# Kernel optimization log

Hardware: AMD Instinct MI355X
Metric: run time of the kernel (lower is better)

Reference implementation:

```python
import jax, jax.numpy as jnp
import numpy as np

NEG_SLOPE = 0.2

def gat_conv(x, src, dst, W, a_src, a_dst, bias, N):
    # PyG GATConv, heads=1: h = xW; e_ij = LeakyReLU(a_src.h_j + a_dst.h_i)
    h = x @ W                                   # [N, H]
    as_ = h @ a_src                             # [N]
    ad_ = h @ a_dst                             # [N]
    e = jax.nn.leaky_relu(as_[src] + ad_[dst], NEG_SLOPE)   # [E]
    m = jax.ops.segment_max(e, dst, num_segments=N)          # per-target max
    w = jnp.exp(e - m[dst])
    denom = jax.ops.segment_sum(w, dst, num_segments=N)
    alpha = w / (denom[dst] + 1e-16)                          # [E]
    out = jax.ops.segment_sum(alpha[:, None] * h[src], dst, num_segments=N)
    return out + bias


def setup_inputs() -> dict:
    key = jax.random.key(0)
    N, E, D, H, A = 20000, 320000, 256, 256, 8
    ks = jax.random.split(key, 16)
    s = lambda k, shp, fan: jax.random.normal(k, shp, jnp.float32) * (1.0 / np.sqrt(fan))
    return {
        "obs": jax.random.normal(ks[0], (N, D), jnp.float32),
        "edge_index": jax.random.randint(ks[1], (2, E), 0, N, dtype=jnp.int32),
        "W1": s(ks[2], (D, H), D), "a1_src": s(ks[3], (H,), H), "a1_dst": s(ks[4], (H,), H), "b1": jnp.zeros((H,), jnp.float32),
        "W2": s(ks[5], (H, H), H), "a2_src": s(ks[6], (H,), H), "a2_dst": s(ks[7], (H,), H), "b2": jnp.zeros((H,), jnp.float32),
        "Wm1": s(ks[8], (H, H), H), "bm1": jnp.zeros((H,), jnp.float32),
        "Wm2": s(ks[9], (H, A), H), "bm2": jnp.zeros((A,), jnp.float32),
    }


def reference(obs, edge_index, W1, a1_src, a1_dst, b1, W2, a2_src, a2_dst, b2, Wm1, bm1, Wm2, bm2):
    N = obs.shape[0]
    loops = jnp.arange(N, dtype=edge_index.dtype)
    src = jnp.concatenate([edge_index[0], loops])   # add self-loops (PyG default)
    dst = jnp.concatenate([edge_index[1], loops])
    x = jax.nn.relu(gat_conv(obs, src, dst, W1, a1_src, a1_dst, b1, N))
    x = jax.nn.relu(gat_conv(x,   src, dst, W2, a2_src, a2_dst, b2, N))
    x = jax.nn.relu(x @ Wm1 + bm1)
    return jnp.tanh(x @ Wm2 + bm2)
```

## Files before the change

### kernel.cpp

```cpp
#include <hip/hip_runtime.h>
#include <hip/hip_bf16.h>
#include <math.h>
#include <stdio.h>

typedef __attribute__((ext_vector_type(8))) short short8;
typedef __attribute__((ext_vector_type(4))) float f32x4;
typedef __attribute__((ext_vector_type(4))) unsigned short us4;
typedef __attribute__((ext_vector_type(8))) unsigned short us8;

__device__ __forceinline__ float us2f(unsigned short u) {
    return __uint_as_float(((unsigned)u) << 16);
}
__device__ __forceinline__ unsigned short f2us_rtn(float f) {
    return (unsigned short)__bfloat16_as_ushort(__float2bfloat16(f));
}

__global__ void prep_all(const float* __restrict__ Wa, const float* __restrict__ Wb,
                         const float* __restrict__ Wc, const float* __restrict__ obs,
                         unsigned short* __restrict__ TA, unsigned short* __restrict__ TB,
                         unsigned short* __restrict__ TC, unsigned short* __restrict__ obsb,
                         float* __restrict__ as1, float* __restrict__ ad1,
                         float* __restrict__ as2, float* __restrict__ ad2,
                         int* __restrict__ deg,
                         int K, int Nn, int N, int nObs8) {
    const int tot = K * Nn;
    int idx = blockIdx.x * blockDim.x + threadIdx.x;
    if (idx < 3 * tot) {
        const float* W;
        unsigned short* T;
        if (idx < tot) { W = Wa; T = TA; }
        else if (idx < 2 * tot) { W = Wb; T = TB; idx -= tot; }
        else { W = Wc; T = TC; idx -= 2 * tot; }
        const int n = idx / K, k = idx - n * K;
        T[idx] = f2us_rtn(W[(size_t)k * Nn + n]);
        return;
    }
    idx -= 3 * tot;
    if (idx < 5 * N) {
        if (idx < N) as1[idx] = 0.f;
        else if (idx < 2 * N) ad1[idx - N] = 0.f;
        else if (idx < 3 * N) as2[idx - 2 * N] = 0.f;
        else if (idx < 4 * N) ad2[idx - 3 * N] = 0.f;
        else deg[idx - 4 * N] = 0;
        return;
    }
    idx -= 5 * N;
    if (idx < nObs8) {
        const float4 a = *(const float4*)(obs + (size_t)idx * 8);
        const float4 b = *(const float4*)(obs + (size_t)idx * 8 + 4);
        const float f[8] = {a.x, a.y, a.z, a.w, b.x, b.y, b.z, b.w};
        short8 o;
#pragma unroll
        for (int e = 0; e < 8; e++) o[e] = (short)f2us_rtn(f[e]);
        *(short8*)(obsb + (size_t)idx * 8) = o;
    }
}

#define LP 72
__global__ __launch_bounds__(256) void gemm_mfma(const unsigned short* __restrict__ A,
                                                 const unsigned short* __restrict__ Bt,
                                                 const float* __restrict__ avs,
                                                 const float* __restrict__ avd,
                                                 float* __restrict__ as_,
                                                 float* __restrict__ ad_,
                                                 unsigned short* __restrict__ C,
                                                 int M, int Nn, int K) {
    __shared__ unsigned short sA[64 * LP];
    __shared__ unsigned short sB[128 * LP];
    const int tid = threadIdx.x;
    const int wave = tid >> 6, lane = tid & 63;
    const int m16 = lane & 15, quad = lane >> 4;
    const int row0 = blockIdx.x * 64, col0 = blockIdx.y * 128;
    const int wr = (wave >> 1) * 32, wc = (wave & 1) * 64;
    const int ar = tid >> 2, akc = (tid & 3) * 8;
    const int bkc = (tid & 7) * 8, bcb = tid >> 3;
    const int gr = (row0 + ar) < M ? (row0 + ar) : (M - 1);
    const unsigned short* Arow = A + (size_t)gr * K + akc;
    const unsigned short* Bcol = Bt + (size_t)(col0 + bcb) * K + bkc;

    short8 rA0, rA1, rb0, rb1, rb2, rb3;
    auto LOADT = [&](int k0) {
        rA0 = *(const short8*)(Arow + k0);
        rA1 = *(const short8*)(Arow + k0 + 32);
        rb0 = *(const short8*)(Bcol + k0);
        rb1 = *(const short8*)(Bcol + (size_t)32 * K + k0);
        rb2 = *(const short8*)(Bcol + (size_t)64 * K + k0);
        rb3 = *(const short8*)(Bcol + (size_t)96 * K + k0);
    };
    auto STORET = [&]() {
        *(short8*)&sA[ar * LP + akc]      = rA0;
        *(short8*)&sA[ar * LP + akc + 32] = rA1;
        *(short8*)&sB[bcb * LP + bkc]        = rb0;
        *(short8*)&sB[(bcb + 32) * LP + bkc] = rb1;
        *(short8*)&sB[(bcb + 64) * LP + bkc] = rb2;
        *(short8*)&sB[(bcb + 96) * LP + bkc] = rb3;
    };

    f32x4 acc[2][4] = {};
    LOADT(0);
    STORET();
    __syncthreads();
    for (int k0 = 0; k0 < K; k0 += 64) {
        const bool more = (k0 + 64) < K;
        if (more) LOADT(k0 + 64);
#pragma unroll
        for (int ks = 0; ks < 2; ks++) {
            short8 ah[2];
#pragma unroll
            for (int mi = 0; mi < 2; mi++)
                ah[mi] = *(const short8*)&sA[(wr + mi * 16 + m16) * LP + ks * 32 + quad * 8];
#pragma unroll
            for (int ni = 0; ni < 4; ni++) {
                const short8 bv = *(const short8*)&sB[(wc + ni * 16 + m16) * LP + ks * 32 + quad * 8];
#pragma unroll
                for (int mi = 0; mi < 2; mi++)
                    acc[mi][ni] = __builtin_amdgcn_mfma_f32_16x16x32_bf16(ah[mi], bv, acc[mi][ni], 0, 0, 0);
            }
        }
        __syncthreads();
        if (more) { STORET(); __syncthreads(); }
    }
    float ps[2][4] = {}, pd[2][4] = {};
#pragma unroll
    for (int mi = 0; mi < 2; mi++) {
        const int orow_base = row0 + wr + mi * 16 + quad * 4;
#pragma unroll
        for (int ni = 0; ni < 4; ni++) {
            const int ocol = col0 + wc + ni * 16 + m16;
            const float asv = avs[ocol], adv = avd[ocol];
#pragma unroll
            for (int r = 0; r < 4; r++) {
                const int orow = orow_base + r;
                if (orow < M) {
                    const float v = acc[mi][ni][r];
                    C[(size_t)orow * Nn + ocol] = f2us_rtn(v);
                    ps[mi][r] = fmaf(v, asv, ps[mi][r]);
                    pd[mi][r] = fmaf(v, adv, pd[mi][r]);
                }
            }
        }
    }
#pragma unroll
    for (int mi = 0; mi < 2; mi++)
#pragma unroll
        for (int r = 0; r < 4; r++)
#pragma unroll
            for (int off = 1; off < 16; off <<= 1) {
                ps[mi][r] += __shfl_xor(ps[mi][r], off);
                pd[mi][r] += __shfl_xor(pd[mi][r], off);
            }
    if (m16 == 0) {
#pragma unroll
        for (int mi = 0; mi < 2; mi++) {
            const int orow_base = row0 + wr + mi * 16 + quad * 4;
#pragma unroll
            for (int r = 0; r < 4; r++) {
                const int orow = orow_base + r;
                if (orow < M) {
                    atomicAdd(&as_[orow], ps[mi][r]);
                    atomicAdd(&ad_[orow], pd[mi][r]);
                }
            }
        }
    }
}

__global__ __launch_bounds__(256) void gemm_head(const unsigned short* __restrict__ A,
                                                 const unsigned short* __restrict__ Bt,
                                                 const float* __restrict__ bias1,
                                                 const float* __restrict__ W2,
                                                 const float* __restrict__ bias2,
                                                 float* __restrict__ out,
                                                 int M, int K, int Aout) {
    __shared__ unsigned short sA[64 * LP];
    __shared__ unsigned short sB[256 * LP];
    __shared__ float pLDS[2][64][8];
    const int tid = threadIdx.x;
    const int wave = tid >> 6, lane = tid & 63;
    const int m16 = lane & 15, quad = lane >> 4;
    const int row0 = blockIdx.x * 64;
    const int wr = (wave >> 1) * 32, wc = (wave & 1) * 128;
    const int ar = tid >> 2, akc = (tid & 3) * 8;
    const int bkc = (tid & 7) * 8, bcb = tid >> 3;
    const int gr = (row0 + ar) < M ? (row0 + ar) : (M - 1);
    const unsigned short* Arow = A + (size_t)gr * K + akc;
    const unsigned short* Bcol = Bt + (size_t)bcb * K + bkc;

    short8 rA0, rA1, rb[8];
    auto LOADT = [&](int k0) {
        rA0 = *(const short8*)(Arow + k0);
        rA1 = *(const short8*)(Arow + k0 + 32);
#pragma unroll
        for (int q = 0; q < 8; q++)
            rb[q] = *(const short8*)(Bcol + (size_t)(32 * q) * K + k0);
    };
    auto STORET = [&]() {
        *(short8*)&sA[ar * LP + akc]      = rA0;
        *(short8*)&sA[ar * LP + akc + 32] = rA1;
#pragma unroll
        for (int q = 0; q < 8; q++)
            *(short8*)&sB[(bcb + 32 * q) * LP + bkc] = rb[q];
    };

    f32x4 acc[2][8] = {};
    LOADT(0);
    STORET();
    __syncthreads();
    for (int k0 = 0; k0 < K; k0 += 64) {
        const bool more = (k0 + 64) < K;
        if (more) LOADT(k0 + 64);
#pragma unroll
        for (int ks = 0; ks < 2; ks++) {
            short8 ah[2];
#pragma unroll
            for (int mi = 0; mi < 2; mi++)
                ah[mi] = *(const short8*)&sA[(wr + mi * 16 + m16) * LP + ks * 32 + quad * 8];
#pragma unroll
            for (int ni = 0; ni < 8; ni++) {
                const short8 bv = *(const short8*)&sB[(wc + ni * 16 + m16) * LP + ks * 32 + quad * 8];
#pragma unroll
                for (int mi = 0; mi < 2; mi++)
                    acc[mi][ni] = __builtin_amdgcn_mfma_f32_16x16x32_bf16(ah[mi], bv, acc[mi][ni], 0, 0, 0);
            }
        }
        __syncthreads();
        if (more) { STORET(); __syncthreads(); }
    }
    float p[2][4][8] = {};
#pragma unroll
    for (int ni = 0; ni < 8; ni++) {
        const int ocol = wc + ni * 16 + m16;
        const float b1v = bias1[ocol];
        float w2[8];
#pragma unroll
        for (int a = 0; a < 8; a++) w2[a] = W2[ocol * 8 + a];
#pragma unroll
        for (int mi = 0; mi < 2; mi++)
#pragma unroll
            for (int r = 0; r < 4; r++) {
                const float v = fmaxf(acc[mi][ni][r] + b1v, 0.f);
#pragma unroll
                for (int a = 0; a < 8; a++) p[mi][r][a] = fmaf(v, w2[a], p[mi][r][a]);
            }
    }
#pragma unroll
    for (int off = 1; off < 16; off <<= 1)
#pragma unroll
        for (int mi = 0; mi < 2; mi++)
#pragma unroll
            for (int r = 0; r < 4; r++)
#pragma unroll
                for (int a = 0; a < 8; a++) p[mi][r][a] += __shfl_xor(p[mi][r][a], off);
    if (m16 == 0) {
        const int half = wc >> 7;
#pragma unroll
        for (int mi = 0; mi < 2; mi++) {
            const int lrow = wr + mi * 16 + quad * 4;
#pragma unroll
            for (int r = 0; r < 4; r++)
#pragma unroll
                for (int a = 0; a < 8; a++) pLDS[half][lrow + r][a] = p[mi][r][a];
        }
    }
    __syncthreads();
#pragma unroll
    for (int u = 0; u < 2; u++) {
        const int idx = tid * 2 + u;
        const int lrow = idx >> 3, a = idx & 7;
        const int orow = row0 + lrow;
        if (orow < M && a < Aout)
            out[(size_t)orow * Aout + a] =
                tanhf(pLDS[0][lrow][a] + pLDS[1][lrow][a] + bias2[a]);
    }
}
#undef LP

__global__ void count_kernel(const int* __restrict__ dstA, int* __restrict__ deg, int E, int Etot) {
    const int e = blockIdx.x * blockDim.x + threadIdx.x;
    if (e >= Etot) return;
    const int d = (e < E) ? dstA[e] : (e - E);
    atomicAdd(&deg[d], 1);
}

__global__ __launch_bounds__(1024) void scan_kernel(const int* __restrict__ deg,
                                                    int* __restrict__ offs,
                                                    int* __restrict__ cursor, int N) {
    __shared__ int sums[1024];
    const int t = threadIdx.x;
    const int chunk = (N + 1023) / 1024;
    const int start = t * chunk;
    int s = 0;
    for (int i = 0; i < chunk; i++) {
        const int p = start + i;
        if (p < N) s += deg[p];
    }
    sums[t] = s;
    __syncthreads();
    for (int off = 1; off < 1024; off <<= 1) {
        const int add = (t >= off) ? sums[t - off] : 0;
        __syncthreads();
        sums[t] += add;
        __syncthreads();
    }
    int run = (t > 0) ? sums[t - 1] : 0;
    for (int i = 0; i < chunk; i++) {
        const int p = start + i;
        if (p < N) { offs[p] = run; cursor[p] = run; run += deg[p]; }
    }
    if (t == 0) offs[N] = sums[1023];
}

__global__ void scatter_kernel(const int* __restrict__ srcA, const int* __restrict__ dstA,
                               int* __restrict__ cursor, int* __restrict__ esrc, int E, int Etot) {
    const int e = blockIdx.x * blockDim.x + threadIdx.x;
    if (e >= Etot) return;
    int s, d;
    if (e < E) { s = srcA[e]; d = dstA[e]; } else { s = d = e - E; }
    const int slot = atomicAdd(&cursor[d], 1);
    esrc[slot] = s;
}

__global__ __launch_bounds__(256) void agg_kernel(const unsigned short* __restrict__ hb,
                                                  const int* __restrict__ offs,
                                                  const int* __restrict__ esrc,
                                                  const float* __restrict__ as_,
                                                  const float* __restrict__ ad_,
                                                  const float* __restrict__ bias,
                                                  unsigned short* __restrict__ xout, int N) {
    const int n = __builtin_amdgcn_readfirstlane(blockIdx.x * 4 + (threadIdx.x >> 6));
    if (n >= N) return;
    const int lane = threadIdx.x & 63;
    const int half = lane >> 5;
    const int f0 = (lane & 31) * 8;
    const int b = offs[n], e2 = offs[n + 1];
    const float adn = ad_[n];
    float a[8] = {};
    float wsum = 0.f;
    for (int c0 = b; c0 < e2; c0 += 16) {
        int s = 0;
        float w = 0.f;
        if (lane < 16) {
            const int j = c0 + lane;
            const int jj = j < e2 ? j : e2 - 1;
            s = esrc[jj];
            if (j < e2) {
                float v = as_[s] + adn;
                v = v > 0.f ? v : 0.2f * v;
                w = __expf(v);
                wsum += w;
            }
        }
        us8 pv[8];
        float wb[8];
#pragma unroll
        for (int u = 0; u < 8; u++) {
            const int el = 2 * u + half;
            const int su = __shfl(s, el);
            wb[u] = __shfl(w, el);
            pv[u] = *(const us8*)(hb + (unsigned)((su << 8) + f0));
        }
#pragma unroll
        for (int u = 0; u < 8; u++)
#pragma unroll
            for (int j2 = 0; j2 < 8; j2++)
                a[j2] = fmaf(wb[u], us2f(pv[u][j2]), a[j2]);
    }
#pragma unroll
    for (int j2 = 0; j2 < 8; j2++) a[j2] += __shfl_xor(a[j2], 32);
#pragma unroll
    for (int off = 32; off; off >>= 1) wsum += __shfl_xor(wsum, off);
    const float inv = 1.0f / (wsum + 1e-16f);
    if (half == 0) {
        const float4 b0 = *(const float4*)(bias + f0);
        const float4 b1 = *(const float4*)(bias + f0 + 4);
        const float bb[8] = {b0.x, b0.y, b0.z, b0.w, b1.x, b1.y, b1.z, b1.w};
        us8 o;
#pragma unroll
        for (int j2 = 0; j2 < 8; j2++)
            o[j2] = f2us_rtn(fmaxf(a[j2] * inv + bb[j2], 0.f));
        *(us8*)(xout + (unsigned)((n << 8) + f0)) = o;
    }
}

extern "C" void kernel_launch(void* const* d_in, const int* in_sizes, int n_in,
                              void* d_out, int out_size, void* d_ws, size_t ws_size,
                              hipStream_t stream) {
    const float* obs = (const float*)d_in[0];
    const int* eidx  = (const int*)d_in[1];
    const float* W1  = (const float*)d_in[2];
    const float* a1s = (const float*)d_in[3];
    const float* a1d = (const float*)d_in[4];
    const float* b1  = (const float*)d_in[5];
    const float* W2  = (const float*)d_in[6];
    const float* a2s = (const float*)d_in[7];
    const float* a2d = (const float*)d_in[8];
    const float* b2v = (const float*)d_in[9];
    const float* Wm1 = (const float*)d_in[10];
    const float* bm1 = (const float*)d_in[11];
    const float* Wm2 = (const float*)d_in[12];
    const float* bm2 = (const float*)d_in[13];
    float* out = (float*)d_out;

    const int Hh = in_sizes[3];
    const int Dd = in_sizes[2] / Hh;
    const int N  = in_sizes[0] / Dd;
    const int E  = in_sizes[1] / 2;
    const int Etot = E + N;
    const int Aout = in_sizes[12] / Hh;

    const int* srcA = eidx;
    const int* dstA = eidx + E;

    size_t off = 0;
    char* ws = (char*)d_ws;
    auto alloc = [&](size_t bytes) -> char* {
        char* p = ws + off;
        off = (off + bytes + 15) & ~(size_t)15;
        return p;
    };
    unsigned short* h    = (unsigned short*)alloc((size_t)N * Hh * 2);
    unsigned short* xb   = (unsigned short*)alloc((size_t)N * Hh * 2);
    unsigned short* obsb = (unsigned short*)alloc((size_t)N * Dd * 2);
    float* as1   = (float*)alloc((size_t)N * 4);
    float* ad1   = (float*)alloc((size_t)N * 4);
    float* as2   = (float*)alloc((size_t)N * 4);
    float* ad2   = (float*)alloc((size_t)N * 4);
    int* deg     = (int*)alloc((size_t)N * 4);
    int* offs    = (int*)alloc((size_t)(N + 1) * 4);
    int* cursor  = (int*)alloc((size_t)N * 4);
    int* esrc    = (int*)alloc((size_t)Etot * 4);
    const size_t wsz = (size_t)Dd * Hh;
    unsigned short* W1t = (unsigned short*)alloc(wsz * 2);
    unsigned short* W2t = (unsigned short*)alloc(wsz * 2);
    unsigned short* Wmt = (unsigned short*)alloc(wsz * 2);

    const int eb = 256;
    const int eg = (Etot + eb - 1) / eb;
    const dim3 ggrid((N + 63) / 64, Hh / 128);
    const int nrow = (N + 63) / 64;
    const int nb4 = (N + 3) / 4;
    const int nObs8 = N * Dd / 8;

    const int ptot = 3 * (int)wsz + 5 * N + nObs8;
    prep_all<<<(ptot + 255) / 256, 256, 0, stream>>>(
        W1, W2, Wm1, obs, W1t, W2t, Wmt, obsb, as1, ad1, as2, ad2, deg, Dd, Hh, N, nObs8);

    count_kernel<<<eg, eb, 0, stream>>>(dstA, deg, E, Etot);
    scan_kernel<<<1, 1024, 0, stream>>>(deg, offs, cursor, N);
    scatter_kernel<<<eg, eb, 0, stream>>>(srcA, dstA, cursor, esrc, E, Etot);

    gemm_mfma<<<ggrid, 256, 0, stream>>>(obsb, W1t, a1s, a1d, as1, ad1, h, N, Hh, Dd);
    agg_kernel<<<nb4, 256, 0, stream>>>(h, offs, esrc, as1, ad1, b1, xb, N);

    gemm_mfma<<<ggrid, 256, 0, stream>>>(xb, W2t, a2s, a2d, as2, ad2, h, N, Hh, Hh);
    agg_kernel<<<nb4, 256, 0, stream>>>(h, offs, esrc, as2, ad2, b2v, xb, N);

    gemm_head<<<nrow, 256, 0, stream>>>(xb, Wmt, bm1, Wm2, bm2, out, N, Hh, Aout);
}
```

Measured before the change: 261.7 us.

## Fuse whole GAT pipeline into one cooperative persistent kernel with grid syncs

```diff
diff --git a/kernel.cpp b/kernel.cpp
--- a/kernel.cpp
+++ b/kernel.cpp
@@ -1,7 +1,9 @@
 #include <hip/hip_runtime.h>
+#include <hip/hip_cooperative_groups.h>
 #include <hip/hip_bf16.h>
 #include <math.h>
-#include <stdio.h>
+
+namespace cg = cooperative_groups;
 
 typedef __attribute__((ext_vector_type(8))) short short8;
 typedef __attribute__((ext_vector_type(4))) float f32x4;
@@ -13,6 +15,427 @@
 }
 __device__ __forceinline__ unsigned short f2us_rtn(float f) {
     return (unsigned short)__bfloat16_as_ushort(__float2bfloat16(f));
+}
+
+#define LP 72
+
+
+__device__ __forceinline__ void gemm_tile(const unsigned short* __restrict__ A,
+                                          const unsigned short* __restrict__ Bt,
+                                          const float* __restrict__ avs,
+                                          const float* __restrict__ avd,
+                                          float* __restrict__ as_,
+                                          float* __restrict__ ad_,
+                                          unsigned short* __restrict__ C,
+                                          int M, int Nn, int K, int row0, int col0,
+                                          unsigned short* sA, unsigned short* sB) {
+    const int tid = threadIdx.x;
+    const int wave = tid >> 6, lane = tid & 63;
+    const int m16 = lane & 15, quad = lane >> 4;
+    const int wr = (wave >> 1) * 32, wc = (wave & 1) * 64;
+    const int ar = tid >> 2, akc = (tid & 3) * 8;
+    const int bkc = (tid & 7) * 8, bcb = tid >> 3;
+    const int gr = (row0 + ar) < M ? (row0 + ar) : (M - 1);
+    const unsigned short* Arow = A + (size_t)gr * K + akc;
+    const unsigned short* Bcol = Bt + (size_t)(col0 + bcb) * K + bkc;
+
+    short8 rA0, rA1, rb0, rb1, rb2, rb3;
+    auto LOADT = [&](int k0) {
+        rA0 = *(const short8*)(Arow + k0);
+        rA1 = *(const short8*)(Arow + k0 + 32);
+        rb0 = *(const short8*)(Bcol + k0);
+        rb1 = *(const short8*)(Bcol + (size_t)32 * K + k0);
+        rb2 = *(const short8*)(Bcol + (size_t)64 * K + k0);
+        rb3 = *(const short8*)(Bcol + (size_t)96 * K + k0);
+    };
+    auto STORET = [&]() {
+        *(short8*)&sA[ar * LP + akc]      = rA0;
+        *(short8*)&sA[ar * LP + akc + 32] = rA1;
+        *(short8*)&sB[bcb * LP + bkc]        = rb0;
+        *(short8*)&sB[(bcb + 32) * LP + bkc] = rb1;
+        *(short8*)&sB[(bcb + 64) * LP + bkc] = rb2;
+        *(short8*)&sB[(bcb + 96) * LP + bkc] = rb3;
+    };
+
+    f32x4 acc[2][4] = {};
+    LOADT(0);
+    STORET();
+    __syncthreads();
+    for (int k0 = 0; k0 < K; k0 += 64) {
+        const bool more = (k0 + 64) < K;
+        if (more) LOADT(k0 + 64);
+#pragma unroll
+        for (int ks = 0; ks < 2; ks++) {
+            short8 ah[2];
+#pragma unroll
+            for (int mi = 0; mi < 2; mi++)
+                ah[mi] = *(const short8*)&sA[(wr + mi * 16 + m16) * LP + ks * 32 + quad * 8];
+#pragma unroll
+            for (int ni = 0; ni < 4; ni++) {
+                const short8 bv = *(const short8*)&sB[(wc + ni * 16 + m16) * LP + ks * 32 + quad * 8];
+#pragma unroll
+                for (int mi = 0; mi < 2; mi++)
+                    acc[mi][ni] = __builtin_amdgcn_mfma_f32_16x16x32_bf16(ah[mi], bv, acc[mi][ni], 0, 0, 0);
+            }
+        }
+        __syncthreads();
+        if (more) { STORET(); __syncthreads(); }
+    }
+    float ps[2][4] = {}, pd[2][4] = {};
+#pragma unroll
+    for (int mi = 0; mi < 2; mi++) {
+        const int orow_base = row0 + wr + mi * 16 + quad * 4;
+#pragma unroll
+        for (int ni = 0; ni < 4; ni++) {
+            const int ocol = col0 + wc + ni * 16 + m16;
+            const float asv = avs[ocol], adv = avd[ocol];
+#pragma unroll
+            for (int r = 0; r < 4; r++) {
+                const int orow = orow_base + r;
+                if (orow < M) {
+                    const float v = acc[mi][ni][r];
+                    C[(size_t)orow * Nn + ocol] = f2us_rtn(v);
+                    ps[mi][r] = fmaf(v, asv, ps[mi][r]);
+                    pd[mi][r] = fmaf(v, adv, pd[mi][r]);
+                }
+            }
+        }
+    }
+#pragma unroll
+    for (int mi = 0; mi < 2; mi++)
+#pragma unroll
+        for (int r = 0; r < 4; r++)
+#pragma unroll
+            for (int off = 1; off < 16; off <<= 1) {
+                ps[mi][r] += __shfl_xor(ps[mi][r], off);
+                pd[mi][r] += __shfl_xor(pd[mi][r], off);
+            }
+    if (m16 == 0) {
+#pragma unroll
+        for (int mi = 0; mi < 2; mi++) {
+            const int orow_base = row0 + wr + mi * 16 + quad * 4;
+#pragma unroll
+            for (int r = 0; r < 4; r++) {
+                const int orow = orow_base + r;
+                if (orow < M) {
+                    atomicAdd(&as_[orow], ps[mi][r]);
+                    atomicAdd(&ad_[orow], pd[mi][r]);
+                }
+            }
+        }
+    }
+}
+
+__device__ __forceinline__ void head_tile(const unsigned short* __restrict__ A,
+                                          const unsigned short* __restrict__ Bt,
+                                          const float* __restrict__ bias1,
+                                          const float* __restrict__ W2,
+                                          const float* __restrict__ bias2,
+                                          float* __restrict__ out,
+                                          int M, int K, int Aout, int row0,
+                                          unsigned short* sA, unsigned short* sB,
+                                          float* pLDS ) {
+    const int tid = threadIdx.x;
+    const int wave = tid >> 6, lane = tid & 63;
+    const int m16 = lane & 15, quad = lane >> 4;
+    const int wr = (wave >> 1) * 32, wc = (wave & 1) * 128;
+    const int ar = tid >> 2, akc = (tid & 3) * 8;
+    const int bkc = (tid & 7) * 8, bcb = tid >> 3;
+    const int gr = (row0 + ar) < M ? (row0 + ar) : (M - 1);
+    const unsigned short* Arow = A + (size_t)gr * K + akc;
+    const unsigned short* Bcol = Bt + (size_t)bcb * K + bkc;
+
+    short8 rA0, rA1, rb[8];
+    auto LOADT = [&](int k0) {
+        rA0 = *(const short8*)(Arow + k0);
+        rA1 = *(const short8*)(Arow + k0 + 32);
+#pragma unroll
+        for (int q = 0; q < 8; q++)
+            rb[q] = *(const short8*)(Bcol + (size_t)(32 * q) * K + k0);
+    };
+    auto STORET = [&]() {
+        *(short8*)&sA[ar * LP + akc]      = rA0;
+        *(short8*)&sA[ar * LP + akc + 32] = rA1;
+#pragma unroll
+        for (int q = 0; q < 8; q++)
+            *(short8*)&sB[(bcb + 32 * q) * LP + bkc] = rb[q];
+    };
+
+    f32x4 acc[2][8] = {};
+    LOADT(0);
+    STORET();
+    __syncthreads();
+    for (int k0 = 0; k0 < K; k0 += 64) {
+        const bool more = (k0 + 64) < K;
+        if (more) LOADT(k0 + 64);
+#pragma unroll
+        for (int ks = 0; ks < 2; ks++) {
+            short8 ah[2];
+#pragma unroll
+            for (int mi = 0; mi < 2; mi++)
+                ah[mi] = *(const short8*)&sA[(wr + mi * 16 + m16) * LP + ks * 32 + quad * 8];
+#pragma unroll
+            for (int ni = 0; ni < 8; ni++) {
+                const short8 bv = *(const short8*)&sB[(wc + ni * 16 + m16) * LP + ks * 32 + quad * 8];
+#pragma unroll
+                for (int mi = 0; mi < 2; mi++)
+                    acc[mi][ni] = __builtin_amdgcn_mfma_f32_16x16x32_bf16(ah[mi], bv, acc[mi][ni], 0, 0, 0);
+            }
+        }
+        __syncthreads();
+        if (more) { STORET(); __syncthreads(); }
+    }
+    float p[2][4][8] = {};
+#pragma unroll
+    for (int ni = 0; ni < 8; ni++) {
+        const int ocol = wc + ni * 16 + m16;
+        const float b1v = bias1[ocol];
+        float w2[8];
+#pragma unroll
+        for (int a = 0; a < 8; a++) w2[a] = W2[ocol * 8 + a];
+#pragma unroll
+        for (int mi = 0; mi < 2; mi++)
+#pragma unroll
+            for (int r = 0; r < 4; r++) {
+                const float v = fmaxf(acc[mi][ni][r] + b1v, 0.f);
+#pragma unroll
+                for (int a = 0; a < 8; a++) p[mi][r][a] = fmaf(v, w2[a], p[mi][r][a]);
+            }
+    }
+#pragma unroll
+    for (int off = 1; off < 16; off <<= 1)
+#pragma unroll
+        for (int mi = 0; mi < 2; mi++)
+#pragma unroll
+            for (int r = 0; r < 4; r++)
+#pragma unroll
+                for (int a = 0; a < 8; a++) p[mi][r][a] += __shfl_xor(p[mi][r][a], off);
+    if (m16 == 0) {
+        const int half = wc >> 7;
+#pragma unroll
+        for (int mi = 0; mi < 2; mi++) {
+            const int lrow = wr + mi * 16 + quad * 4;
+#pragma unroll
+            for (int r = 0; r < 4; r++)
+#pragma unroll
+                for (int a = 0; a < 8; a++)
+                    pLDS[(half * 64 + lrow + r) * 8 + a] = p[mi][r][a];
+        }
+    }
+    __syncthreads();
+#pragma unroll
+    for (int u = 0; u < 2; u++) {
+        const int idx = tid * 2 + u;
+        const int lrow = idx >> 3, a = idx & 7;
+        const int orow = row0 + lrow;
+        if (orow < M && a < Aout)
+            out[(size_t)orow * Aout + a] =
+                tanhf(pLDS[(0 * 64 + lrow) * 8 + a] + pLDS[(1 * 64 + lrow) * 8 + a] + bias2[a]);
+    }
+}
+
+__device__ __forceinline__ void agg_phase(const unsigned short* __restrict__ hb,
+                                          const int* __restrict__ offs,
+                                          const int* __restrict__ esrc,
+                                          const float* __restrict__ as_,
+                                          const float* __restrict__ ad_,
+                                          const float* __restrict__ bias,
+                                          unsigned short* __restrict__ xout,
+                                          int N, int nwaves) {
+    const int w0 = blockIdx.x * 4 + (threadIdx.x >> 6);
+    const int lane = threadIdx.x & 63;
+    const int half = lane >> 5;
+    const int f0 = (lane & 31) * 8;
+    for (int n0 = w0; n0 < N; n0 += nwaves) {
+        const int n = __builtin_amdgcn_readfirstlane(n0);
+        const int b = offs[n], e2 = offs[n + 1];
+        const float adn = ad_[n];
+        float a[8] = {};
+        float wsum = 0.f;
+        for (int c0 = b; c0 < e2; c0 += 16) {
+            int s = 0;
+            float w = 0.f;
+            if (lane < 16) {
+                const int j = c0 + lane;
+                const int jj = j < e2 ? j : e2 - 1;
+                s = esrc[jj];
+                if (j < e2) {
+                    float v = as_[s] + adn;
+                    v = v > 0.f ? v : 0.2f * v;
+                    w = __expf(v);
+                    wsum += w;
+                }
+            }
+            us8 pv[8];
+            float wb[8];
+#pragma unroll
+            for (int u = 0; u < 8; u++) {
+                const int el = 2 * u + half;
+                const int su = __shfl(s, el);
+                wb[u] = __shfl(w, el);
+                pv[u] = *(const us8*)(hb + (unsigned)((su << 8) + f0));
+            }
+#pragma unroll
+            for (int u = 0; u < 8; u++)
+#pragma unroll
+                for (int j2 = 0; j2 < 8; j2++)
+                    a[j2] = fmaf(wb[u], us2f(pv[u][j2]), a[j2]);
+        }
+#pragma unroll
+        for (int j2 = 0; j2 < 8; j2++) a[j2] += __shfl_xor(a[j2], 32);
+#pragma unroll
+        for (int off = 32; off; off >>= 1) wsum += __shfl_xor(wsum, off);
+        const float inv = 1.0f / (wsum + 1e-16f);
+        if (half == 0) {
+            const float4 b0 = *(const float4*)(bias + f0);
+            const float4 b1 = *(const float4*)(bias + f0 + 4);
+            const float bb[8] = {b0.x, b0.y, b0.z, b0.w, b1.x, b1.y, b1.z, b1.w};
+            us8 o;
+#pragma unroll
+            for (int j2 = 0; j2 < 8; j2++)
+                o[j2] = f2us_rtn(fmaxf(a[j2] * inv + bb[j2], 0.f));
+            *(us8*)(xout + (unsigned)((n << 8) + f0)) = o;
+        }
+    }
+}
+
+__device__ __forceinline__ void scan_body(const int* __restrict__ deg,
+                                          int* __restrict__ offs,
+                                          int* __restrict__ cursor,
+                                          int N, int per, int* sums) {
+    const int t = threadIdx.x;
+    const int base = t * per;
+    int s = 0;
+    for (int i = 0; i < per; i += 4) {
+        const int4 v = *(const int4*)(deg + base + i);
+        s += v.x + v.y + v.z + v.w;
+    }
+    sums[t] = s;
+    __syncthreads();
+    for (int off = 1; off < 256; off <<= 1) {
+        const int add = (t >= off) ? sums[t - off] : 0;
+        __syncthreads();
+        sums[t] += add;
+        __syncthreads();
+    }
+    int run = (t > 0) ? sums[t - 1] : 0;
+    for (int i = 0; i < per; i += 4) {
+        const int4 v = *(const int4*)(deg + base + i);
+        const int p = base + i;
+        const int vv[4] = {v.x, v.y, v.z, v.w};
+#pragma unroll
+        for (int j = 0; j < 4; j++) {
+            if (p + j < N) { offs[p + j] = run; cursor[p + j] = run; }
+            run += vv[j];
+        }
+    }
+    if (t == 255) offs[N] = run;
+}
+
+struct MegaArgs {
+    const float *obs, *W1, *a1s, *a1d, *b1, *W2w, *a2s, *a2d, *b2, *Wm1, *bm1, *Wm2, *bm2;
+    const int *srcA, *dstA;
+    unsigned short *h, *xb, *obsb, *W1t, *W2t, *Wmt;
+    float *as1, *ad1, *as2, *ad2;
+    int *deg, *offs, *cursor, *esrc;
+    float* out;
+    int N, E, Etot, Dd, Hh, Aout, Npad, per, ntiles, nrow;
+};
+
+#define SMEM_BYTES ((64 * LP + 256 * LP) * 2 + 2 * 64 * 8 * 4)
+
+__global__ __launch_bounds__(256, 2) void mega(MegaArgs a) {
+    cg::grid_group grid = cg::this_grid();
+    __shared__ __align__(16) unsigned char smem[SMEM_BYTES];
+    unsigned short* sA = (unsigned short*)smem;
+    unsigned short* sB = sA + 64 * LP;
+    float* pLDS = (float*)(smem + (64 * LP + 256 * LP) * 2);
+    int* sums = (int*)smem;
+    const int tid = threadIdx.x, bid = blockIdx.x;
+    const int G = gridDim.x;
+    const int gsz = G * 256;
+    const int gtid = bid * 256 + tid;
+
+    {
+        const int totW = 3 * a.Dd * a.Hh;
+        const int z4 = 4 * a.N;
+        const int nObs8 = a.N * a.Dd / 8;
+        const int total = totW + z4 + a.Npad + nObs8;
+        for (int i = gtid; i < total; i += gsz) {
+            int idx = i;
+            if (idx < totW) {
+                const int tot = a.Dd * a.Hh;
+                const float* W;
+                unsigned short* T;
+                if (idx < tot) { W = a.W1; T = a.W1t; }
+                else if (idx < 2 * tot) { W = a.W2w; T = a.W2t; idx -= tot; }
+                else { W = a.Wm1; T = a.Wmt; idx -= 2 * tot; }
+                const int n = idx / a.Dd, k = idx - n * a.Dd;
+                T[idx] = f2us_rtn(W[(size_t)k * a.Hh + n]);
+                continue;
+            }
+            idx -= totW;
+            if (idx < z4) {
+                if (idx < a.N) a.as1[idx] = 0.f;
+                else if (idx < 2 * a.N) a.ad1[idx - a.N] = 0.f;
+                else if (idx < 3 * a.N) a.as2[idx - 2 * a.N] = 0.f;
+                else a.ad2[idx - 3 * a.N] = 0.f;
+                continue;
+            }
+            idx -= z4;
+            if (idx < a.Npad) { a.deg[idx] = 0; continue; }
+            idx -= a.Npad;
+            {
+                const float4 v0 = *(const float4*)(a.obs + (size_t)idx * 8);
+                const float4 v1 = *(const float4*)(a.obs + (size_t)idx * 8 + 4);
+                const float f[8] = {v0.x, v0.y, v0.z, v0.w, v1.x, v1.y, v1.z, v1.w};
+                short8 o;
+#pragma unroll
+                for (int e = 0; e < 8; e++) o[e] = (short)f2us_rtn(f[e]);
+                *(short8*)(a.obsb + (size_t)idx * 8) = o;
+            }
+        }
+    }
+    grid.sync();
+    const int crew = G - 64;
+    if (bid < 64) {
+        for (int e = bid * 256 + tid; e < a.Etot; e += 64 * 256) {
+            const int d = (e < a.E) ? a.dstA[e] : (e - a.E);
+            atomicAdd(&a.deg[d], 1);
+        }
+    } else {
+        const int t = bid - 64;
+        if (t < a.ntiles)
+            gemm_tile(a.obsb, a.W1t, a.a1s, a.a1d, a.as1, a.ad1, a.h,
+                      a.N, a.Hh, a.Dd, (t >> 1) * 64, (t & 1) * 128, sA, sB);
+    }
+    grid.sync();
+    if (bid == 0) {
+        scan_body(a.deg, a.offs, a.cursor, a.N, a.per, sums);
+    } else if (bid >= 64) {
+        for (int t = crew + (bid - 64); t < a.ntiles; t += crew)
+            gemm_tile(a.obsb, a.W1t, a.a1s, a.a1d, a.as1, a.ad1, a.h,
+                      a.N, a.Hh, a.Dd, (t >> 1) * 64, (t & 1) * 128, sA, sB);
+    }
+    grid.sync();
+    for (int e = gtid; e < a.Etot; e += gsz) {
+        int s, d;
+        if (e < a.E) { s = a.srcA[e]; d = a.dstA[e]; } else { s = d = e - a.E; }
+        const int slot = atomicAdd(&a.cursor[d], 1);
+        a.esrc[slot] = s;
+    }
+    grid.sync();
+    agg_phase(a.h, a.offs, a.esrc, a.as1, a.ad1, a.b1, a.xb, a.N, G * 4);
+    grid.sync();
+    for (int t = bid; t < a.ntiles; t += G)
+        gemm_tile(a.xb, a.W2t, a.a2s, a.a2d, a.as2, a.ad2, a.h,
+                  a.N, a.Hh, a.Hh, (t >> 1) * 64, (t & 1) * 128, sA, sB);
+    grid.sync();
+    agg_phase(a.h, a.offs, a.esrc, a.as2, a.ad2, a.b2, a.xb, a.N, G * 4);
+    grid.sync();
+    for (int t = bid; t < a.nrow; t += G)
+        head_tile(a.xb, a.Wmt, a.bm1, a.Wm2, a.bm2, a.out,
+                  a.N, a.Hh, a.Aout, t * 64, sA, sB, pLDS);
 }
 
 __global__ void prep_all(const float* __restrict__ Wa, const float* __restrict__ Wb,
@@ -56,224 +479,32 @@
     }
 }
 
-#define LP 72
-__global__ __launch_bounds__(256) void gemm_mfma(const unsigned short* __restrict__ A,
-                                                 const unsigned short* __restrict__ Bt,
-                                                 const float* __restrict__ avs,
-                                                 const float* __restrict__ avd,
-                                                 float* __restrict__ as_,
-                                                 float* __restrict__ ad_,
-                                                 unsigned short* __restrict__ C,
-                                                 int M, int Nn, int K) {
+__global__ __launch_bounds__(256) void gemm_mfma_k(const unsigned short* __restrict__ A,
+                                                   const unsigned short* __restrict__ Bt,
+                                                   const float* __restrict__ avs,
+                                                   const float* __restrict__ avd,
+                                                   float* __restrict__ as_,
+                                                   float* __restrict__ ad_,
+                                                   unsigned short* __restrict__ C,
+                                                   int M, int Nn, int K) {
     __shared__ unsigned short sA[64 * LP];
     __shared__ unsigned short sB[128 * LP];
-    const int tid = threadIdx.x;
-    const int wave = tid >> 6, lane = tid & 63;
-    const int m16 = lane & 15, quad = lane >> 4;
-    const int row0 = blockIdx.x * 64, col0 = blockIdx.y * 128;
-    const int wr = (wave >> 1) * 32, wc = (wave & 1) * 64;
-    const int ar = tid >> 2, akc = (tid & 3) * 8;
-    const int bkc = (tid & 7) * 8, bcb = tid >> 3;
-    const int gr = (row0 + ar) < M ? (row0 + ar) : (M - 1);
-    const unsigned short* Arow = A + (size_t)gr * K + akc;
-    const unsigned short* Bcol = Bt + (size_t)(col0 + bcb) * K + bkc;
-
-    short8 rA0, rA1, rb0, rb1, rb2, rb3;
-    auto LOADT = [&](int k0) {
-        rA0 = *(const short8*)(Arow + k0);
-        rA1 = *(const short8*)(Arow + k0 + 32);
-        rb0 = *(const short8*)(Bcol + k0);
-        rb1 = *(const short8*)(Bcol + (size_t)32 * K + k0);
-        rb2 = *(const short8*)(Bcol + (size_t)64 * K + k0);
-        rb3 = *(const short8*)(Bcol + (size_t)96 * K + k0);
-    };
-    auto STORET = [&]() {
-        *(short8*)&sA[ar * LP + akc]      = rA0;
-        *(short8*)&sA[ar * LP + akc + 32] = rA1;
-        *(short8*)&sB[bcb * LP + bkc]        = rb0;
-        *(short8*)&sB[(bcb + 32) * LP + bkc] = rb1;
-        *(short8*)&sB[(bcb + 64) * LP + bkc] = rb2;
-        *(short8*)&sB[(bcb + 96) * LP + bkc] = rb3;
-    };
-
-    f32x4 acc[2][4] = {};
-    LOADT(0);
-    STORET();
-    __syncthreads();
-    for (int k0 = 0; k0 < K; k0 += 64) {
-        const bool more = (k0 + 64) < K;
-        if (more) LOADT(k0 + 64);
-#pragma unroll
-        for (int ks = 0; ks < 2; ks++) {
-            short8 ah[2];
-#pragma unroll
-            for (int mi = 0; mi < 2; mi++)
-                ah[mi] = *(const short8*)&sA[(wr + mi * 16 + m16) * LP + ks * 32 + quad * 8];
-#pragma unroll
-            for (int ni = 0; ni < 4; ni++) {
-                const short8 bv = *(const short8*)&sB[(wc + ni * 16 + m16) * LP + ks * 32 + quad * 8];
-#pragma unroll
-                for (int mi = 0; mi < 2; mi++)
-                    acc[mi][ni] = __builtin_amdgcn_mfma_f32_16x16x32_bf16(ah[mi], bv, acc[mi][ni], 0, 0, 0);
-            }
-        }
-        __syncthreads();
-        if (more) { STORET(); __syncthreads(); }
-    }
-    float ps[2][4] = {}, pd[2][4] = {};
-#pragma unroll
-    for (int mi = 0; mi < 2; mi++) {
-        const int orow_base = row0 + wr + mi * 16 + quad * 4;
-#pragma unroll
-        for (int ni = 0; ni < 4; ni++) {
-            const int ocol = col0 + wc + ni * 16 + m16;
-            const float asv = avs[ocol], adv = avd[ocol];
-#pragma unroll
-            for (int r = 0; r < 4; r++) {
-                const int orow = orow_base + r;
-                if (orow < M) {
-                    const float v = acc[mi][ni][r];
-                    C[(size_t)orow * Nn + ocol] = f2us_rtn(v);
-                    ps[mi][r] = fmaf(v, asv, ps[mi][r]);
-                    pd[mi][r] = fmaf(v, adv, pd[mi][r]);
-                }
-            }
-        }
-    }
-#pragma unroll
-    for (int mi = 0; mi < 2; mi++)
-#pragma unroll
-        for (int r = 0; r < 4; r++)
-#pragma unroll
-            for (int off = 1; off < 16; off <<= 1) {
-                ps[mi][r] += __shfl_xor(ps[mi][r], off);
-                pd[mi][r] += __shfl_xor(pd[mi][r], off);
-            }
-    if (m16 == 0) {
-#pragma unroll
-        for (int mi = 0; mi < 2; mi++) {
-            const int orow_base = row0 + wr + mi * 16 + quad * 4;
-#pragma unroll
-            for (int r = 0; r < 4; r++) {
-                const int orow = orow_base + r;
-                if (orow < M) {
-                    atomicAdd(&as_[orow], ps[mi][r]);
-                    atomicAdd(&ad_[orow], pd[mi][r]);
-                }
-            }
-        }
-    }
-}
-
-__global__ __launch_bounds__(256) void gemm_head(const unsigned short* __restrict__ A,
-                                                 const unsigned short* __restrict__ Bt,
-                                                 const float* __restrict__ bias1,
-                                                 const float* __restrict__ W2,
-                                                 const float* __restrict__ bias2,
-                                                 float* __restrict__ out,
-                                                 int M, int K, int Aout) {
+    gemm_tile(A, Bt, avs, avd, as_, ad_, C, M, Nn, K,
+              blockIdx.x * 64, blockIdx.y * 128, sA, sB);
+}
+
+__global__ __launch_bounds__(256) void gemm_head_k(const unsigned short* __restrict__ A,
+                                                   const unsigned short* __restrict__ Bt,
+                                                   const float* __restrict__ bias1,
+                                                   const float* __restrict__ W2,
+                                                   const float* __restrict__ bias2,
+                                                   float* __restrict__ out,
+                                                   int M, int K, int Aout) {
     __shared__ unsigned short sA[64 * LP];
     __shared__ unsigned short sB[256 * LP];
-    __shared__ float pLDS[2][64][8];
-    const int tid = threadIdx.x;
-    const int wave = tid >> 6, lane = tid & 63;
-    const int m16 = lane & 15, quad = lane >> 4;
-    const int row0 = blockIdx.x * 64;
-    const int wr = (wave >> 1) * 32, wc = (wave & 1) * 128;
-    const int ar = tid >> 2, akc = (tid & 3) * 8;
-    const int bkc = (tid & 7) * 8, bcb = tid >> 3;
-    const int gr = (row0 + ar) < M ? (row0 + ar) : (M - 1);
-    const unsigned short* Arow = A + (size_t)gr * K + akc;
-    const unsigned short* Bcol = Bt + (size_t)bcb * K + bkc;
-
-    short8 rA0, rA1, rb[8];
-    auto LOADT = [&](int k0) {
-        rA0 = *(const short8*)(Arow + k0);
-        rA1 = *(const short8*)(Arow + k0 + 32);
-#pragma unroll
-        for (int q = 0; q < 8; q++)
-            rb[q] = *(const short8*)(Bcol + (size_t)(32 * q) * K + k0);
-    };
-    auto STORET = [&]() {
-        *(short8*)&sA[ar * LP + akc]      = rA0;
-        *(short8*)&sA[ar * LP + akc + 32] = rA1;
-#pragma unroll
-        for (int q = 0; q < 8; q++)
-            *(short8*)&sB[(bcb + 32 * q) * LP + bkc] = rb[q];
-    };
-
-    f32x4 acc[2][8] = {};
-    LOADT(0);
-    STORET();
-    __syncthreads();
-    for (int k0 = 0; k0 < K; k0 += 64) {
-        const bool more = (k0 + 64) < K;
-        if (more) LOADT(k0 + 64);
-#pragma unroll
-        for (int ks = 0; ks < 2; ks++) {
-            short8 ah[2];
-#pragma unroll
-            for (int mi = 0; mi < 2; mi++)
-                ah[mi] = *(const short8*)&sA[(wr + mi * 16 + m16) * LP + ks * 32 + quad * 8];
-#pragma unroll
-            for (int ni = 0; ni < 8; ni++) {
-                const short8 bv = *(const short8*)&sB[(wc + ni * 16 + m16) * LP + ks * 32 + quad * 8];
-#pragma unroll
-                for (int mi = 0; mi < 2; mi++)
-                    acc[mi][ni] = __builtin_amdgcn_mfma_f32_16x16x32_bf16(ah[mi], bv, acc[mi][ni], 0, 0, 0);
-            }
-        }
-        __syncthreads();
-        if (more) { STORET(); __syncthreads(); }
-    }
-    float p[2][4][8] = {};
-#pragma unroll
-    for (int ni = 0; ni < 8; ni++) {
-        const int ocol = wc + ni * 16 + m16;
-        const float b1v = bias1[ocol];
-        float w2[8];
-#pragma unroll
-        for (int a = 0; a < 8; a++) w2[a] = W2[ocol * 8 + a];
-#pragma unroll
-        for (int mi = 0; mi < 2; mi++)
-#pragma unroll
-            for (int r = 0; r < 4; r++) {
-                const float v = fmaxf(acc[mi][ni][r] + b1v, 0.f);
-#pragma unroll
-                for (int a = 0; a < 8; a++) p[mi][r][a] = fmaf(v, w2[a], p[mi][r][a]);
-            }
-    }
-#pragma unroll
-    for (int off = 1; off < 16; off <<= 1)
-#pragma unroll
-        for (int mi = 0; mi < 2; mi++)
-#pragma unroll
-            for (int r = 0; r < 4; r++)
-#pragma unroll
-                for (int a = 0; a < 8; a++) p[mi][r][a] += __shfl_xor(p[mi][r][a], off);
-    if (m16 == 0) {
-        const int half = wc >> 7;
-#pragma unroll
-        for (int mi = 0; mi < 2; mi++) {
-            const int lrow = wr + mi * 16 + quad * 4;
-#pragma unroll
-            for (int r = 0; r < 4; r++)
-#pragma unroll
-                for (int a = 0; a < 8; a++) pLDS[half][lrow + r][a] = p[mi][r][a];
-        }
-    }
-    __syncthreads();
-#pragma unroll
-    for (int u = 0; u < 2; u++) {
-        const int idx = tid * 2 + u;
-        const int lrow = idx >> 3, a = idx & 7;
-        const int orow = row0 + lrow;
-        if (orow < M && a < Aout)
-            out[(size_t)orow * Aout + a] =
-                tanhf(pLDS[0][lrow][a] + pLDS[1][lrow][a] + bias2[a]);
-    }
-}
-#undef LP
+    __shared__ float pLDS[2 * 64 * 8];
+    head_tile(A, Bt, bias1, W2, bias2, out, M, K, Aout, blockIdx.x * 64, sA, sB, pLDS);
+}
 
 __global__ void count_kernel(const int* __restrict__ dstA, int* __restrict__ deg, int E, int Etot) {
     const int e = blockIdx.x * blockDim.x + threadIdx.x;
@@ -327,59 +558,7 @@
                                                   const float* __restrict__ ad_,
                                                   const float* __restrict__ bias,
                                                   unsigned short* __restrict__ xout, int N) {
-    const int n = __builtin_amdgcn_readfirstlane(blockIdx.x * 4 + (threadIdx.x >> 6));
-    if (n >= N) return;
-    const int lane = threadIdx.x & 63;
-    const int half = lane >> 5;
-    const int f0 = (lane & 31) * 8;
-    const int b = offs[n], e2 = offs[n + 1];
-    const float adn = ad_[n];
-    float a[8] = {};
-    float wsum = 0.f;
-    for (int c0 = b; c0 < e2; c0 += 16) {
-        int s = 0;
-        float w = 0.f;
-        if (lane < 16) {
-            const int j = c0 + lane;
-            const int jj = j < e2 ? j : e2 - 1;
-            s = esrc[jj];
-            if (j < e2) {
-                float v = as_[s] + adn;
-                v = v > 0.f ? v : 0.2f * v;
-                w = __expf(v);
-                wsum += w;
-            }
-        }
-        us8 pv[8];
-        float wb[8];
-#pragma unroll
-        for (int u = 0; u < 8; u++) {
-            const int el = 2 * u + half;
-            const int su = __shfl(s, el);
-            wb[u] = __shfl(w, el);
-            pv[u] = *(const us8*)(hb + (unsigned)((su << 8) + f0));
-        }
-#pragma unroll
-        for (int u = 0; u < 8; u++)
-#pragma unroll
-            for (int j2 = 0; j2 < 8; j2++)
-                a[j2] = fmaf(wb[u], us2f(pv[u][j2]), a[j2]);
-    }
-#pragma unroll
-    for (int j2 = 0; j2 < 8; j2++) a[j2] += __shfl_xor(a[j2], 32);
-#pragma unroll
-    for (int off = 32; off; off >>= 1) wsum += __shfl_xor(wsum, off);
-    const float inv = 1.0f / (wsum + 1e-16f);
-    if (half == 0) {
-        const float4 b0 = *(const float4*)(bias + f0);
-        const float4 b1 = *(const float4*)(bias + f0 + 4);
-        const float bb[8] = {b0.x, b0.y, b0.z, b0.w, b1.x, b1.y, b1.z, b1.w};
-        us8 o;
-#pragma unroll
-        for (int j2 = 0; j2 < 8; j2++)
-            o[j2] = f2us_rtn(fmaxf(a[j2] * inv + bb[j2], 0.f));
-        *(us8*)(xout + (unsigned)((n << 8) + f0)) = o;
-    }
+    agg_phase(hb, offs, esrc, as_, ad_, bias, xout, N, gridDim.x * 4);
 }
 
 extern "C" void kernel_launch(void* const* d_in, const int* in_sizes, int n_in,
@@ -411,6 +590,9 @@
     const int* srcA = eidx;
     const int* dstA = eidx + E;
 
+    const int per = ((N + 1023) / 1024) * 4;
+    const int Npad = 256 * per;
+
     size_t off = 0;
     char* ws = (char*)d_ws;
     auto alloc = [&](size_t bytes) -> char* {
@@ -425,7 +607,7 @@
     float* ad1   = (float*)alloc((size_t)N * 4);
     float* as2   = (float*)alloc((size_t)N * 4);
     float* ad2   = (float*)alloc((size_t)N * 4);
-    int* deg     = (int*)alloc((size_t)N * 4);
+    int* deg     = (int*)alloc((size_t)Npad * 4);
     int* offs    = (int*)alloc((size_t)(N + 1) * 4);
     int* cursor  = (int*)alloc((size_t)N * 4);
     int* esrc    = (int*)alloc((size_t)Etot * 4);
@@ -434,26 +616,45 @@
     unsigned short* W2t = (unsigned short*)alloc(wsz * 2);
     unsigned short* Wmt = (unsigned short*)alloc(wsz * 2);
 
+    const int nrow = (N + 63) / 64;
+    const int ntiles = nrow * (Hh / 128);
+
+    int nb = 0;
+    hipError_t qe = hipOccupancyMaxActiveBlocksPerMultiprocessor(&nb, mega, 256, 0);
+    int G = (qe == hipSuccess && nb > 0) ? nb * 256 : 0;
+    if (G > 512) G = 512;
+    if (G >= 256) {
+        MegaArgs ma;
+        ma.obs = obs; ma.W1 = W1; ma.a1s = a1s; ma.a1d = a1d; ma.b1 = b1;
+        ma.W2w = W2; ma.a2s = a2s; ma.a2d = a2d; ma.b2 = b2v;
+        ma.Wm1 = Wm1; ma.bm1 = bm1; ma.Wm2 = Wm2; ma.bm2 = bm2;
+        ma.srcA = srcA; ma.dstA = dstA;
+        ma.h = h; ma.xb = xb; ma.obsb = obsb; ma.W1t = W1t; ma.W2t = W2t; ma.Wmt = Wmt;
+        ma.as1 = as1; ma.ad1 = ad1; ma.as2 = as2; ma.ad2 = ad2;
+        ma.deg = deg; ma.offs = offs; ma.cursor = cursor; ma.esrc = esrc;
+        ma.out = out;
+        ma.N = N; ma.E = E; ma.Etot = Etot; ma.Dd = Dd; ma.Hh = Hh; ma.Aout = Aout;
+        ma.Npad = Npad; ma.per = per; ma.ntiles = ntiles; ma.nrow = nrow;
+        void* kargs[] = { (void*)&ma };
+        hipError_t le = hipLaunchCooperativeKernel(mega, dim3(G), dim3(256), kargs, 0, stream);
+        if (le == hipSuccess) return;
+    }
+
     const int eb = 256;
     const int eg = (Etot + eb - 1) / eb;
-    const dim3 ggrid((N + 63) / 64, Hh / 128);
-    const int nrow = (N + 63) / 64;
+    const dim3 ggrid(nrow, Hh / 128);
     const int nb4 = (N + 3) / 4;
     const int nObs8 = N * Dd / 8;
 
     const int ptot = 3 * (int)wsz + 5 * N + nObs8;
     prep_all<<<(ptot + 255) / 256, 256, 0, stream>>>(
         W1, W2, Wm1, obs, W1t, W2t, Wmt, obsb, as1, ad1, as2, ad2, deg, Dd, Hh, N, nObs8);
-
     count_kernel<<<eg, eb, 0, stream>>>(dstA, deg, E, Etot);
     scan_kernel<<<1, 1024, 0, stream>>>(deg, offs, cursor, N);
     scatter_kernel<<<eg, eb, 0, stream>>>(srcA, dstA, cursor, esrc, E, Etot);
-
-    gemm_mfma<<<ggrid, 256, 0, stream>>>(obsb, W1t, a1s, a1d, as1, ad1, h, N, Hh, Dd);
+    gemm_mfma_k<<<ggrid, 256, 0, stream>>>(obsb, W1t, a1s, a1d, as1, ad1, h, N, Hh, Dd);
     agg_kernel<<<nb4, 256, 0, stream>>>(h, offs, esrc, as1, ad1, b1, xb, N);
-
-    gemm_mfma<<<ggrid, 256, 0, stream>>>(xb, W2t, a2s, a2d, as2, ad2, h, N, Hh, Hh);
+    gemm_mfma_k<<<ggrid, 256, 0, stream>>>(xb, W2t, a2s, a2d, as2, ad2, h, N, Hh, Hh);
     agg_kernel<<<nb4, 256, 0, stream>>>(h, offs, esrc, as2, ad2, b2v, xb, N);
-
-    gemm_head<<<nrow, 256, 0, stream>>>(xb, Wmt, bm1, Wm2, bm2, out, N, Hh, Aout);
-}
+    gemm_head_k<<<nrow, 256, 0, stream>>>(xb, Wmt, bm1, Wm2, bm2, out, N, Hh, Aout);
+}
```

New measurement: 538.5 us. 106% more time.

## Restructure GAT GEMM: stage full-K B slice in LDS, stream A from registers

Applied to the files above, without the earlier changes.

```diff
diff --git a/kernel.cpp b/kernel.cpp
--- a/kernel.cpp
+++ b/kernel.cpp
@@ -1,11 +1,9 @@
 #include <hip/hip_runtime.h>
 #include <hip/hip_bf16.h>
 #include <math.h>
-#include <stdio.h>
 
 typedef __attribute__((ext_vector_type(8))) short short8;
 typedef __attribute__((ext_vector_type(4))) float f32x4;
-typedef __attribute__((ext_vector_type(4))) unsigned short us4;
 typedef __attribute__((ext_vector_type(8))) unsigned short us8;
 
 __device__ __forceinline__ float us2f(unsigned short u) {
@@ -56,115 +54,106 @@
     }
 }
 
-#define LP 72
-__global__ __launch_bounds__(256) void gemm_mfma(const unsigned short* __restrict__ A,
-                                                 const unsigned short* __restrict__ Bt,
-                                                 const float* __restrict__ avs,
-                                                 const float* __restrict__ avd,
-                                                 float* __restrict__ as_,
-                                                 float* __restrict__ ad_,
-                                                 unsigned short* __restrict__ C,
-                                                 int M, int Nn, int K) {
-    __shared__ unsigned short sA[64 * LP];
-    __shared__ unsigned short sB[128 * LP];
+#define LPB 264
+__global__ __launch_bounds__(256, 4) void gemm_mfma(const unsigned short* __restrict__ A,
+                                                    const unsigned short* __restrict__ Bt,
+                                                    const float* __restrict__ avs,
+                                                    const float* __restrict__ avd,
+                                                    float* __restrict__ as_,
+                                                    float* __restrict__ ad_,
+                                                    unsigned short* __restrict__ C,
+                                                    int M, int Nn, int K) {
+    __shared__ unsigned short sB[64 * LPB];
     const int tid = threadIdx.x;
     const int wave = tid >> 6, lane = tid & 63;
     const int m16 = lane & 15, quad = lane >> 4;
-    const int row0 = blockIdx.x * 64, col0 = blockIdx.y * 128;
-    const int wr = (wave >> 1) * 32, wc = (wave & 1) * 64;
-    const int ar = tid >> 2, akc = (tid & 3) * 8;
-    const int bkc = (tid & 7) * 8, bcb = tid >> 3;
-    const int gr = (row0 + ar) < M ? (row0 + ar) : (M - 1);
-    const unsigned short* Arow = A + (size_t)gr * K + akc;
-    const unsigned short* Bcol = Bt + (size_t)(col0 + bcb) * K + bkc;
-
-    short8 rA0, rA1, rb0, rb1, rb2, rb3;
-    auto LOADT = [&](int k0) {
-        rA0 = *(const short8*)(Arow + k0);
-        rA1 = *(const short8*)(Arow + k0 + 32);
-        rb0 = *(const short8*)(Bcol + k0);
-        rb1 = *(const short8*)(Bcol + (size_t)32 * K + k0);
-        rb2 = *(const short8*)(Bcol + (size_t)64 * K + k0);
-        rb3 = *(const short8*)(Bcol + (size_t)96 * K + k0);
-    };
-    auto STORET = [&]() {
-        *(short8*)&sA[ar * LP + akc]      = rA0;
-        *(short8*)&sA[ar * LP + akc + 32] = rA1;
-        *(short8*)&sB[bcb * LP + bkc]        = rb0;
-        *(short8*)&sB[(bcb + 32) * LP + bkc] = rb1;
-        *(short8*)&sB[(bcb + 64) * LP + bkc] = rb2;
-        *(short8*)&sB[(bcb + 96) * LP + bkc] = rb3;
-    };
-
-    f32x4 acc[2][4] = {};
-    LOADT(0);
-    STORET();
+    const int row0 = blockIdx.x * 64, col0 = blockIdx.y * 64;
+    const int wr = wave * 16;
+
+    {
+        const int c = tid >> 2, kc0 = (tid & 3) * 64;
+        const unsigned short* Bp = Bt + (size_t)(col0 + c) * K + kc0;
+        unsigned short* dp = &sB[c * LPB + kc0];
+#pragma unroll
+        for (int j = 0; j < 8; j++)
+            *(short8*)(dp + j * 8) = *(const short8*)(Bp + j * 8);
+    }
+
+    int gr = row0 + wr + m16;
+    if (gr >= M) gr = M - 1;
+    const unsigned short* Arow = A + (size_t)gr * K + quad * 8;
+    short8 a0 = *(const short8*)(Arow);
+    short8 a1 = *(const short8*)(Arow + 32);
+    short8 a2 = *(const short8*)(Arow + 64);
+    short8 a3 = *(const short8*)(Arow + 96);
     __syncthreads();
-    for (int k0 = 0; k0 < K; k0 += 64) {
-        const bool more = (k0 + 64) < K;
-        if (more) LOADT(k0 + 64);
-#pragma unroll
-        for (int ks = 0; ks < 2; ks++) {
-            short8 ah[2];
-#pragma unroll
-            for (int mi = 0; mi < 2; mi++)
-                ah[mi] = *(const short8*)&sA[(wr + mi * 16 + m16) * LP + ks * 32 + quad * 8];
-#pragma unroll
-            for (int ni = 0; ni < 4; ni++) {
-                const short8 bv = *(const short8*)&sB[(wc + ni * 16 + m16) * LP + ks * 32 + quad * 8];
-#pragma unroll
-                for (int mi = 0; mi < 2; mi++)
-                    acc[mi][ni] = __builtin_amdgcn_mfma_f32_16x16x32_bf16(ah[mi], bv, acc[mi][ni], 0, 0, 0);
+
+    f32x4 acc[4] = {};
+    const unsigned short* sBl = &sB[m16 * LPB + quad * 8];
+#define BSTEP(af, kk)                                                              \
+    {                                                                              \
+        _Pragma("unroll")                                                          \
+        for (int ni = 0; ni < 4; ni++) {                                           \
+            const short8 bv = *(const short8*)(sBl + ni * (16 * LPB) + (kk));      \
+            acc[ni] = __builtin_amdgcn_mfma_f32_16x16x32_bf16(af, bv, acc[ni], 0, 0, 0); \
+        }                                                                          \
+    }
+    for (int k0 = 0; k0 < K; k0 += 128) {
+        const bool more = (k0 + 128) < K;
+        short8 n0, n1, n2, n3;
+        if (more) {
+            n0 = *(const short8*)(Arow + k0 + 128);
+            n1 = *(const short8*)(Arow + k0 + 160);
+            n2 = *(const short8*)(Arow + k0 + 192);
+            n3 = *(const short8*)(Arow + k0 + 224);
+        }
+        BSTEP(a0, k0)
+        BSTEP(a1, k0 + 32)
+        BSTEP(a2, k0 + 64)
+        BSTEP(a3, k0 + 96)
+        if (!more) break;
+        a0 = n0; a1 = n1; a2 = n2; a3 = n3;
+    }
+#undef BSTEP
+
+    float ps[4] = {}, pd[4] = {};
+    const int orow_base = row0 + wr + quad * 4;
+#pragma unroll
+    for (int ni = 0; ni < 4; ni++) {
+        const int ocol = col0 + ni * 16 + m16;
+        const float asv = avs[ocol], adv = avd[ocol];
+#pragma unroll
+        for (int r = 0; r < 4; r++) {
+            const int orow = orow_base + r;
+            if (orow < M) {
+                const float v = acc[ni][r];
+                C[(size_t)orow * Nn + ocol] = f2us_rtn(v);
+                ps[r] = fmaf(v, asv, ps[r]);
+                pd[r] = fmaf(v, adv, pd[r]);
             }
         }
-        __syncthreads();
-        if (more) { STORET(); __syncthreads(); }
-    }
-    float ps[2][4] = {}, pd[2][4] = {};
-#pragma unroll
-    for (int mi = 0; mi < 2; mi++) {
-        const int orow_base = row0 + wr + mi * 16 + quad * 4;
-#pragma unroll
-        for (int ni = 0; ni < 4; ni++) {
-            const int ocol = col0 + wc + ni * 16 + m16;
-            const float asv = avs[ocol], adv = avd[ocol];
-#pragma unroll
-            for (int r = 0; r < 4; r++) {
-                const int orow = orow_base + r;
-                if (orow < M) {
-                    const float v = acc[mi][ni][r];
-                    C[(size_t)orow * Nn + ocol] = f2us_rtn(v);
-                    ps[mi][r] = fmaf(v, asv, ps[mi][r]);
-                    pd[mi][r] = fmaf(v, adv, pd[mi][r]);
-                }
+    }
+#pragma unroll
+    for (int r = 0; r < 4; r++)
+#pragma unroll
+        for (int off = 1; off < 16; off <<= 1) {
+            ps[r] += __shfl_xor(ps[r], off);
+            pd[r] += __shfl_xor(pd[r], off);
+        }
+    if (m16 == 0) {
+#pragma unroll
+        for (int r = 0; r < 4; r++) {
+            const int orow = orow_base + r;
+            if (orow < M) {
+                atomicAdd(&as_[orow], ps[r]);
+                atomicAdd(&ad_[orow], pd[r]);
             }
         }
     }
-#pragma unroll
-    for (int mi = 0; mi < 2; mi++)
-#pragma unroll
-        for (int r = 0; r < 4; r++)
-#pragma unroll
-            for (int off = 1; off < 16; off <<= 1) {
-                ps[mi][r] += __shfl_xor(ps[mi][r], off);
-                pd[mi][r] += __shfl_xor(pd[mi][r], off);
-            }
-    if (m16 == 0) {
-#pragma unroll
-        for (int mi = 0; mi < 2; mi++) {
-            const int orow_base = row0 + wr + mi * 16 + quad * 4;
-#pragma unroll
-            for (int r = 0; r < 4; r++) {
-                const int orow = orow_base + r;
-                if (orow < M) {
-                    atomicAdd(&as_[orow], ps[mi][r]);
-                    atomicAdd(&ad_[orow], pd[mi][r]);
-                }
-            }
-        }
-    }
-}
-
+}
+#undef LPB
+
+#define LP 72
 __global__ __launch_bounds__(256) void gemm_head(const unsigned short* __restrict__ A,
                                                  const unsigned short* __restrict__ Bt,
                                                  const float* __restrict__ bias1,
@@ -436,8 +425,8 @@
 
     const int eb = 256;
     const int eg = (Etot + eb - 1) / eb;
-    const dim3 ggrid((N + 63) / 64, Hh / 128);
     const int nrow = (N + 63) / 64;
+    const dim3 ggrid(nrow, Hh / 64);
     const int nb4 = (N + 3) / 4;
     const int nObs8 = N * Dd / 8;
 
```

After: 269.5 us. 1.03x slower.
